# Performance work log

Measured on AMD Instinct MI355X. Metric: run time of the kernel, lower is better.

The kernel has to match this reference:

```python
import jax, jax.numpy as jnp
import numpy as np

FIELD = 32
DIM = 64
LAYER_SIZE = (128, 128)


def setup_inputs() -> dict:
    key = jax.random.key(0)
    ks = jax.random.split(key, 5)
    B = 4096
    x = jax.random.normal(ks[0], (B, FIELD, DIM), dtype=jnp.float32)
    # conv1d kernel-size-1 weights, stored as [out_channels, in_channels]
    field_nums = [FIELD]
    params = {}
    for i, size in enumerate(LAYER_SIZE):
        in_ch = field_nums[-1] * field_nums[0]
        fan = 1.0 / np.sqrt(in_ch)
        params[f"w{i}"] = jax.random.uniform(ks[1 + 2 * i % 4], (size, in_ch), minval=-fan, maxval=fan, dtype=jnp.float32)
        params[f"b{i}"] = jax.random.uniform(ks[2 + 2 * i % 4], (size,), minval=-fan, maxval=fan, dtype=jnp.float32)
        field_nums.append(size // 2)
    return {"cin_inputs": x, "w0": params["w0"], "b0": params["b0"], "w1": params["w1"], "b1": params["b1"]}


def _cin(x, weights, biases):
    # x: [B, F, D]
    B, F, D = x.shape
    hidden = x
    finals = []
    n_layers = len(weights)
    for i, (w, b) in enumerate(zip(weights, biases)):
        size = w.shape[0]
        # outer product over field dims: [B, H, F, D] -> reshape to [B, H*F, D]
        z = jnp.einsum('bhd,bfd->bhfd', hidden, x).reshape(B, hidden.shape[1] * F, D)
        # 1x1 conv over channel dim == per-position matmul
        y = jnp.einsum('bcd,oc->bod', z, w) + b[None, :, None]
        y = jax.nn.relu(y)
        if i != n_layers - 1:
            hidden, direct = y[:, : size // 2, :], y[:, size // 2 :, :]
        else:
            direct = y
        finals.append(direct)
    return jnp.concatenate(finals, axis=1).sum(-1)  # [B, out_dim]


def reference(cin_inputs, w0, b0, w1, b1):
    return _cin(cin_inputs, [w0, w1], [b0, b1])
```

## Files before the change

### kernel.cpp

```cpp
#include <hip/hip_runtime.h>
#include <hip/hip_fp16.h>


typedef __attribute__((ext_vector_type(8))) _Float16 f16x8;
typedef __attribute__((ext_vector_type(4))) float f32x4;
typedef __attribute__((ext_vector_type(4))) unsigned short us4;
typedef unsigned short ushortT;

__global__ void cin_pack_w(const float* __restrict__ w0,
                           const float* __restrict__ w1,
                           ushortT* __restrict__ wp) {
    int gidx = blockIdx.x * 256 + threadIdx.x;
    if (gidx >= 49152) return;
    const float* src;
    ushortT* dst;
    if (gidx < 16384) {
        int kk = gidx >> 9, rem = gidx & 511;
        int n = rem >> 6, lp = rem & 63;
        int o = n * 16 + (lp & 15);
        int c = kk * 32 + ((lp >> 4) << 3);
        src = w0 + o * 1024 + c;
        dst = wp + gidx * 8;
    } else {
        int g1 = gidx - 16384;
        int kk = g1 >> 9, rem = g1 & 511;
        int n = rem >> 6, lp = rem & 63;
        int o = n * 16 + (lp & 15);
        int c = kk * 32 + ((lp >> 4) << 3);
        src = w1 + o * 2048 + c;
        dst = wp + 131072 + g1 * 8;
    }
    ushortT tmp[8];
#pragma unroll
    for (int j = 0; j < 8; ++j) {
        __half h = __float2half(src[j]);
        tmp[j] = __builtin_bit_cast(ushortT, h);
    }
    *reinterpret_cast<f16x8*>(dst) = *reinterpret_cast<const f16x8*>(tmp);
}

__global__ __launch_bounds__(256, 2) void cin_mfma_kernel(
    const float* __restrict__ x,
    const float* __restrict__ b0,
    const float* __restrict__ b1,
    const ushortT* __restrict__ wp,
    float* __restrict__ out)
{
    const int tid = threadIdx.x;
    const int l   = tid & 63;
    const int w   = tid >> 6;
    const int b   = blockIdx.x * 4 + w;
    const int r16 = l & 15;
    const int g   = l >> 4;

    __shared__ ushortT Xh[4][2048];
    __shared__ ushortT Hsm[4][64 * 66];
    __shared__ __align__(16) ushortT Wb[2][4096];

    ushortT* Xw = Xh[w];
    ushortT* Hw = Hsm[w];

    const float* xb = x + (size_t)b * 2048;
#pragma unroll
    for (int i = 0; i < 8; ++i) {
        float4 v = reinterpret_cast<const float4*>(xb)[i * 64 + l];
        int flat = (i * 64 + l) * 4;
        us4 h;
        h[0] = __builtin_bit_cast(ushortT, __float2half(v.x));
        h[1] = __builtin_bit_cast(ushortT, __float2half(v.y));
        h[2] = __builtin_bit_cast(ushortT, __float2half(v.z));
        h[3] = __builtin_bit_cast(ushortT, __float2half(v.w));
        *reinterpret_cast<us4*>(&Xw[flat]) = h;
    }

    {
        const char* src = (const char*)wp + (size_t)(w * 2) * 1024 + (size_t)l * 16;
        __builtin_amdgcn_global_load_lds((const unsigned int*)src,
                                         (unsigned int*)&Wb[0][(w * 2) * 512], 16, 0, 0);
        __builtin_amdgcn_global_load_lds((const unsigned int*)(src + 1024),
                                         (unsigned int*)&Wb[0][(w * 2 + 1) * 512], 16, 0, 0);
    }
    __syncthreads();

    __half2 tf16[4][4];
#pragma unroll
    for (int mt = 0; mt < 4; ++mt)
#pragma unroll
        for (int p = 0; p < 4; ++p) {
            unsigned lo = Xw[(g * 8 + 2 * p) * 64 + mt * 16 + r16];
            unsigned hi = Xw[(g * 8 + 2 * p + 1) * 64 + mt * 16 + r16];
            tf16[mt][p] = __builtin_bit_cast(__half2, lo | (hi << 16));
        }

    f32x4 acc[4][8];
#pragma unroll
    for (int mt = 0; mt < 4; ++mt)
#pragma unroll
        for (int n = 0; n < 8; ++n) acc[mt][n] = (f32x4){0.f, 0.f, 0.f, 0.f};

#pragma unroll 1
    for (int ktg = 0; ktg < 96; ++ktg) {
        const int buf = ktg & 1;

        if (ktg + 1 < 96) {
            const char* src = (const char*)wp + (size_t)(ktg + 1) * 8192 +
                              (size_t)(w * 2) * 1024 + (size_t)l * 16;
            __builtin_amdgcn_global_load_lds((const unsigned int*)src,
                (unsigned int*)&Wb[buf ^ 1][(w * 2) * 512], 16, 0, 0);
            __builtin_amdgcn_global_load_lds((const unsigned int*)(src + 1024),
                (unsigned int*)&Wb[buf ^ 1][(w * 2 + 1) * 512], 16, 0, 0);
        }

        __half2 th[4];
        if (ktg < 32) {
#pragma unroll
            for (int mt = 0; mt < 4; ++mt) {
                unsigned u = Xw[ktg * 64 + mt * 16 + r16];
                th[mt] = __builtin_bit_cast(__half2, (u << 16) | u);
            }
        } else {
#pragma unroll
            for (int mt = 0; mt < 4; ++mt) {
                unsigned u = Hw[(ktg - 32) * 66 + mt * 16 + r16];
                th[mt] = __builtin_bit_cast(__half2, (u << 16) | u);
            }
        }

        f16x8 Bf[8];
#pragma unroll
        for (int n = 0; n < 8; ++n)
            Bf[n] = *reinterpret_cast<const f16x8*>(&Wb[buf][n * 512 + l * 8]);

#pragma unroll
        for (int mt = 0; mt < 4; ++mt) {
            union { __half2 h2[4]; f16x8 v; } Af;
#pragma unroll
            for (int p = 0; p < 4; ++p)
                Af.h2[p] = __hmul2(tf16[mt][p], th[mt]);
#pragma unroll
            for (int n = 0; n < 8; ++n)
                acc[mt][n] = __builtin_amdgcn_mfma_f32_16x16x32_f16(
                    Af.v, Bf[n], acc[mt][n], 0, 0, 0);
        }

        __syncthreads();

        if (ktg == 31) {
#pragma unroll
            for (int n = 0; n < 4; ++n) {
                float bn = b0[n * 16 + r16];
#pragma unroll
                for (int mt = 0; mt < 4; ++mt)
#pragma unroll
                    for (int r = 0; r < 4; ++r) {
                        float y = fmaxf(acc[mt][n][r] + bn, 0.f);
                        int d = mt * 16 + g * 4 + r;
                        int o = n * 16 + r16;
                        __half hy = __float2half(y);
                        Hw[o * 66 + d] = __builtin_bit_cast(ushortT, hy);
                    }
            }
#pragma unroll
            for (int n = 4; n < 8; ++n) {
                float bn = b0[n * 16 + r16];
                float s = 0.f;
#pragma unroll
                for (int mt = 0; mt < 4; ++mt)
#pragma unroll
                    for (int r = 0; r < 4; ++r)
                        s += fmaxf(acc[mt][n][r] + bn, 0.f);
                s += __shfl_xor(s, 16);
                s += __shfl_xor(s, 32);
                if (l < 16) out[(size_t)b * 192 + (n - 4) * 16 + l] = s;
            }
#pragma unroll
            for (int mt = 0; mt < 4; ++mt)
#pragma unroll
                for (int n = 0; n < 8; ++n) acc[mt][n] = (f32x4){0.f, 0.f, 0.f, 0.f};
        }
    }

#pragma unroll
    for (int n = 0; n < 8; ++n) {
        float bn = b1[n * 16 + r16];
        float s = 0.f;
#pragma unroll
        for (int mt = 0; mt < 4; ++mt)
#pragma unroll
            for (int r = 0; r < 4; ++r)
                s += fmaxf(acc[mt][n][r] + bn, 0.f);
        s += __shfl_xor(s, 16);
        s += __shfl_xor(s, 32);
        if (l < 16) out[(size_t)b * 192 + 64 + n * 16 + l] = s;
    }
}

__global__ __launch_bounds__(256, 4) void cin_fp32_kernel(
    const float* __restrict__ x, const float* __restrict__ w0,
    const float* __restrict__ b0, const float* __restrict__ w1,
    const float* __restrict__ b1, float* __restrict__ out)
{
    const int b = blockIdx.x;
    const int tid = threadIdx.x;
    const int d = tid & 63;
    const int wave = tid >> 6;

    __shared__ float Xs[32][64];
    __shared__ float Hsf[64][64];

    const float* xb = x + (size_t)b * 2048;
    float treg[32];
#pragma unroll
    for (int f = 0; f < 32; ++f) treg[f] = xb[f * 64 + d];
    if (wave == 0) {
#pragma unroll
        for (int f = 0; f < 32; ++f) Xs[f][d] = treg[f];
    }
    __syncthreads();
    const int o_base = __builtin_amdgcn_readfirstlane(wave * 32);

    for (int oi = 0; oi < 32; ++oi) {
        const int o = o_base + oi;
        const float* wrow = w0 + (size_t)o * 1024;
        float acc = b0[o];
        for (int h = 0; h < 32; ++h) {
            const float* wv = wrow + h * 32;
            const float th = Xs[h][d];
            float s0 = 0.f, s1 = 0.f, s2 = 0.f, s3 = 0.f;
#pragma unroll
            for (int f = 0; f < 32; f += 4) {
                s0 = fmaf(wv[f + 0], treg[f + 0], s0);
                s1 = fmaf(wv[f + 1], treg[f + 1], s1);
                s2 = fmaf(wv[f + 2], treg[f + 2], s2);
                s3 = fmaf(wv[f + 3], treg[f + 3], s3);
            }
            acc = fmaf((s0 + s1) + (s2 + s3), th, acc);
        }
        float y = fmaxf(acc, 0.f);
        if (o < 64) {
            Hsf[o][d] = y;
        } else {
#pragma unroll
            for (int off = 32; off > 0; off >>= 1) y += __shfl_xor(y, off, 64);
            if (d == 0) out[(size_t)b * 192 + (o - 64)] = y;
        }
    }
    __syncthreads();

    for (int oi = 0; oi < 32; ++oi) {
        const int o = o_base + oi;
        const float* wrow = w1 + (size_t)o * 2048;
        float acc = b1[o];
        for (int h = 0; h < 64; ++h) {
            const float* wv = wrow + h * 32;
            const float th = Hsf[h][d];
            float s0 = 0.f, s1 = 0.f, s2 = 0.f, s3 = 0.f;
#pragma unroll
            for (int f = 0; f < 32; f += 4) {
                s0 = fmaf(wv[f + 0], treg[f + 0], s0);
                s1 = fmaf(wv[f + 1], treg[f + 1], s1);
                s2 = fmaf(wv[f + 2], treg[f + 2], s2);
                s3 = fmaf(wv[f + 3], treg[f + 3], s3);
            }
            acc = fmaf((s0 + s1) + (s2 + s3), th, acc);
        }
        float y = fmaxf(acc, 0.f);
#pragma unroll
        for (int off = 32; off > 0; off >>= 1) y += __shfl_xor(y, off, 64);
        if (d == 0) out[(size_t)b * 192 + 64 + o] = y;
    }
}

extern "C" void kernel_launch(void* const* d_in, const int* in_sizes, int n_in,
                              void* d_out, int out_size, void* d_ws, size_t ws_size,
                              hipStream_t stream) {
    const float* x  = (const float*)d_in[0];
    const float* w0 = (const float*)d_in[1];
    const float* b0 = (const float*)d_in[2];
    const float* w1 = (const float*)d_in[3];
    const float* b1 = (const float*)d_in[4];
    float* out = (float*)d_out;

    if (ws_size >= 786432) {
        ushortT* wp = (ushortT*)d_ws;
        cin_pack_w<<<192, 256, 0, stream>>>(w0, w1, wp);
        cin_mfma_kernel<<<1024, 256, 0, stream>>>(x, b0, b1, wp, out);
    } else {
        cin_fp32_kernel<<<4096, 256, 0, stream>>>(x, w0, b0, w1, b1, out);
    }
}
```

Before: 165.8 us.

## Deepen weight prefetch to two stages and register-prefetch next fragments

Preloads the first two weight tiles into both LDS buffers and moves the global-to-LDS prefetch distance from one to two iterations. Inside the loop, the B fragments and the broadcast hidden/input scalars for the next iteration are read into registers right after each MFMA column, so LDS reads overlap the matrix work instead of sitting before it. The aim is to hide LDS and global latency behind MFMA issue. The cost is higher register pressure from carrying next-iteration fragments, plus extra boundary handling at iteration 31 and at the last iteration. The compiler may also insert conservative vmcnt waits that serialise the deeper prefetch.

```diff
diff --git a/kernel.cpp b/kernel.cpp
--- a/kernel.cpp
+++ b/kernel.cpp
@@ -73,12 +73,14 @@
         *reinterpret_cast<us4*>(&Xw[flat]) = h;
     }
 
-    {
-        const char* src = (const char*)wp + (size_t)(w * 2) * 1024 + (size_t)l * 16;
+#pragma unroll
+    for (int c = 0; c < 2; ++c) {
+        const char* src = (const char*)wp + (size_t)c * 8192 +
+                          (size_t)(w * 2) * 1024 + (size_t)l * 16;
         __builtin_amdgcn_global_load_lds((const unsigned int*)src,
-                                         (unsigned int*)&Wb[0][(w * 2) * 512], 16, 0, 0);
+                                         (unsigned int*)&Wb[c][(w * 2) * 512], 16, 0, 0);
         __builtin_amdgcn_global_load_lds((const unsigned int*)(src + 1024),
-                                         (unsigned int*)&Wb[0][(w * 2 + 1) * 512], 16, 0, 0);
+                                         (unsigned int*)&Wb[c][(w * 2 + 1) * 512], 16, 0, 0);
     }
     __syncthreads();
 
@@ -92,6 +94,19 @@
             tf16[mt][p] = __builtin_bit_cast(__half2, lo | (hi << 16));
         }
 
+    __half2 th[4];
+#pragma unroll
+    for (int mt = 0; mt < 4; ++mt) {
+        unsigned u = Xw[mt * 16 + r16];
+        th[mt] = __builtin_bit_cast(__half2, (u << 16) | u);
+    }
+    f16x8 Bf[8];
+#pragma unroll
+    for (int n = 0; n < 8; ++n)
+        Bf[n] = *reinterpret_cast<const f16x8*>(&Wb[0][n * 512 + l * 8]);
+
+    __syncthreads();
+
     f32x4 acc[4][8];
 #pragma unroll
     for (int mt = 0; mt < 4; ++mt)
@@ -99,53 +114,51 @@
         for (int n = 0; n < 8; ++n) acc[mt][n] = (f32x4){0.f, 0.f, 0.f, 0.f};
 
 #pragma unroll 1
-    for (int ktg = 0; ktg < 96; ++ktg) {
-        const int buf = ktg & 1;
-
-        if (ktg + 1 < 96) {
-            const char* src = (const char*)wp + (size_t)(ktg + 1) * 8192 +
+    for (int k = 0; k < 96; ++k) {
+        const int cur = k & 1;
+
+        if (k + 2 < 96) {
+            const char* src = (const char*)wp + (size_t)(k + 2) * 8192 +
                               (size_t)(w * 2) * 1024 + (size_t)l * 16;
             __builtin_amdgcn_global_load_lds((const unsigned int*)src,
-                (unsigned int*)&Wb[buf ^ 1][(w * 2) * 512], 16, 0, 0);
+                (unsigned int*)&Wb[cur][(w * 2) * 512], 16, 0, 0);
             __builtin_amdgcn_global_load_lds((const unsigned int*)(src + 1024),
-                (unsigned int*)&Wb[buf ^ 1][(w * 2 + 1) * 512], 16, 0, 0);
-        }
-
-        __half2 th[4];
-        if (ktg < 32) {
+                (unsigned int*)&Wb[cur][(w * 2 + 1) * 512], 16, 0, 0);
+        }
+
+        const bool pf_th = (k < 95) && (k != 31);
+        const ushortT* WbN = Wb[(k < 95) ? (cur ^ 1) : cur];
+        const ushortT* thp = (k + 1 < 32) ? (Xw + (k + 1) * 64)
+                                          : (Hw + (k - 31) * 66);
+
+        union AfU { __half2 h2[4]; f16x8 v; };
+        AfU Af[4];
+#pragma unroll
+        for (int mt = 0; mt < 4; ++mt)
+#pragma unroll
+            for (int p = 0; p < 4; ++p)
+                Af[mt].h2[p] = __hmul2(tf16[mt][p], th[mt]);
+
+        if (pf_th) {
 #pragma unroll
             for (int mt = 0; mt < 4; ++mt) {
-                unsigned u = Xw[ktg * 64 + mt * 16 + r16];
+                unsigned u = thp[mt * 16 + r16];
                 th[mt] = __builtin_bit_cast(__half2, (u << 16) | u);
             }
-        } else {
-#pragma unroll
-            for (int mt = 0; mt < 4; ++mt) {
-                unsigned u = Hw[(ktg - 32) * 66 + mt * 16 + r16];
-                th[mt] = __builtin_bit_cast(__half2, (u << 16) | u);
-            }
-        }
-
-        f16x8 Bf[8];
-#pragma unroll
-        for (int n = 0; n < 8; ++n)
-            Bf[n] = *reinterpret_cast<const f16x8*>(&Wb[buf][n * 512 + l * 8]);
-
-#pragma unroll
-        for (int mt = 0; mt < 4; ++mt) {
-            union { __half2 h2[4]; f16x8 v; } Af;
-#pragma unroll
-            for (int p = 0; p < 4; ++p)
-                Af.h2[p] = __hmul2(tf16[mt][p], th[mt]);
-#pragma unroll
-            for (int n = 0; n < 8; ++n)
+        }
+
+#pragma unroll
+        for (int n = 0; n < 8; ++n) {
+#pragma unroll
+            for (int mt = 0; mt < 4; ++mt)
                 acc[mt][n] = __builtin_amdgcn_mfma_f32_16x16x32_f16(
-                    Af.v, Bf[n], acc[mt][n], 0, 0, 0);
+                    Af[mt].v, Bf[n], acc[mt][n], 0, 0, 0);
+            Bf[n] = *reinterpret_cast<const f16x8*>(&WbN[n * 512 + l * 8]);
         }
 
         __syncthreads();
 
-        if (ktg == 31) {
+        if (k == 31) {
 #pragma unroll
             for (int n = 0; n < 4; ++n) {
                 float bn = b0[n * 16 + r16];
@@ -177,6 +190,11 @@
             for (int mt = 0; mt < 4; ++mt)
 #pragma unroll
                 for (int n = 0; n < 8; ++n) acc[mt][n] = (f32x4){0.f, 0.f, 0.f, 0.f};
+#pragma unroll
+            for (int mt = 0; mt < 4; ++mt) {
+                unsigned u = Hw[mt * 16 + r16];
+                th[mt] = __builtin_bit_cast(__half2, (u << 16) | u);
+            }
         }
     }
 
```

Measured after the change: 169.1 us. Within noise of the previous version (+2.0%).
